# Performance work log

Measured on AMD Instinct MI355X. Metric: run time of the kernel, lower is better.

## Reference

```python
import jax, jax.numpy as jnp
import numpy as np

B, C, E, L = 128, 128, 10, 16  # atoms, channels, elements, num_ell (lmax=3)
K3_0, K2_0, K1_0 = 23, 4, 1    # num_params per correlation order, 0e output
K3_1, K2_1, K1_1 = 33, 6, 1    # num_params per correlation order, 1o output (num_equiv=3)


def setup_inputs() -> dict:
    key = jax.random.key(0)
    ks = jax.random.split(key, 16)
    inp = {
        'x': jax.random.normal(ks[0], (B, C, L), jnp.float32),
        'y': jax.random.uniform(ks[1], (B, E), jnp.float32),
        # generalized CG (U) buffers -- random dense stand-ins with faithful shapes
        'U1_0e': jax.random.normal(ks[2], (L, K1_0), jnp.float32),
        'U2_0e': jax.random.normal(ks[3], (L, L, K2_0), jnp.float32),
        'U3_0e': jax.random.normal(ks[4], (L, L, L, K3_0), jnp.float32),
        'U1_1o': jax.random.normal(ks[5], (3, L, K1_1), jnp.float32),
        'U2_1o': jax.random.normal(ks[6], (3, L, L, K2_1), jnp.float32),
        'U3_1o': jax.random.normal(ks[7], (3, L, L, L, K3_1), jnp.float32),
        # per-element weights, init randn/num_params as in torch
        'w1_0e': jax.random.normal(ks[8], (E, K1_0, C), jnp.float32) / K1_0,
        'w2_0e': jax.random.normal(ks[9], (E, K2_0, C), jnp.float32) / K2_0,
        'w3_0e': jax.random.normal(ks[10], (E, K3_0, C), jnp.float32) / K3_0,
        'w1_1o': jax.random.normal(ks[11], (E, K1_1, C), jnp.float32) / K1_1,
        'w2_1o': jax.random.normal(ks[12], (E, K2_1, C), jnp.float32) / K2_1,
        'w3_1o': jax.random.normal(ks[13], (E, K3_1, C), jnp.float32) / K3_1,
    }
    return inp


def _contract_0e(x, y, U1, U2, U3, w1, w2, w3):
    # main: 'wxik,ekc,bci,be->bcwx' (explicit path to control peak memory)
    wy3 = jnp.einsum('ekc,be->bkc', w3, y)              # [B,K3,C]
    t = jnp.einsum('wxik,bkc->bcwxi', U3, wy3)          # [B,C,L,L,L]
    out = jnp.einsum('bcwxi,bci->bcwx', t, x)           # [B,C,L,L]
    # order 2: weighting 'wxk,ekc,be->bcwx', features 'bcwi,bci->bcw'
    c2 = jnp.einsum('wxk,ekc,be->bcwx', U2, w2, y)
    out = jnp.einsum('bcwi,bci->bcw', c2 + out, x)
    # order 1: weighting 'wk,ekc,be->bcw', features 'bci,bci->bc'
    c1 = jnp.einsum('wk,ekc,be->bcw', U1, w1, y)
    out = jnp.einsum('bci,bci->bc', c1 + out, x)
    return out  # [B, C]


def _contract_1o(x, y, U1, U2, U3, w1, w2, w3):
    # main: 'wxvik,ekc,bci,be->bcwxv'  (w = equivariance dim of size 3)
    wy3 = jnp.einsum('ekc,be->bkc', w3, y)              # [B,K3,C]
    t = jnp.einsum('wxvik,bkc->bcwxvi', U3, wy3)        # [B,C,3,L,L,L]
    out = jnp.einsum('bcwxvi,bci->bcwxv', t, x)         # [B,C,3,L,L]
    # order 2: 'wxvk,ekc,be->bcwxv' ; features 'bcwxi,bci->bcwx'
    c2 = jnp.einsum('wxvk,ekc,be->bcwxv', U2, w2, y)
    out = jnp.einsum('bcwxi,bci->bcwx', c2 + out, x)
    # order 1: 'wxk,ekc,be->bcwx' ; features 'bcwi,bci->bcw'
    c1 = jnp.einsum('wxk,ekc,be->bcwx', U1, w1, y)
    out = jnp.einsum('bcwi,bci->bcw', c1 + out, x)
    return out.reshape(out.shape[0], -1)  # [B, 3*C]


def reference(x, y, U1_0e, U2_0e, U3_0e, U1_1o, U2_1o, U3_1o,
              w1_0e, w2_0e, w3_0e, w1_1o, w2_1o, w3_1o):
    out0 = _contract_0e(x, y, U1_0e, U2_0e, U3_0e, w1_0e, w2_0e, w3_0e)
    out1 = _contract_1o(x, y, U1_1o, U2_1o, U3_1o, w1_1o, w2_1o, w3_1o)
    return jnp.concatenate([out0, out1], axis=-1)  # [B, C + 3*C]
```

## Files before the change

kernel.cpp:

```cpp
#include <hip/hip_runtime.h>


typedef float  f32x4  __attribute__((ext_vector_type(4)));
typedef short  short8 __attribute__((ext_vector_type(8)));

namespace {
constexpr int EE = 10;

struct Sh1 {
  unsigned short B1[64][552];
  float x[16][64];
  float z[40][64];
  float red[12][64];
};
struct Sh0 {
  unsigned short B0[64][392];
  float x[16][64];
  float z[28][64];
  float red[8][64];
};
union ShU { Sh1 o1; Sh0 o0; };
}

__device__ __forceinline__ unsigned cvtpk(float lo, float hi) {
  unsigned r;
  asm("v_cvt_pk_bf16_f32 %0, %1, %2" : "=v"(r) : "v"(lo), "v"(hi));
  return r;
}

__device__ __forceinline__ short8 pack8(float f0, float f1, float f2, float f3,
                                        float f4, float f5, float f6, float f7) {
  union { short8 s; unsigned u[4]; } r;
  r.u[0] = cvtpk(f0, f1);
  r.u[1] = cvtpk(f2, f3);
  r.u[2] = cvtpk(f4, f5);
  r.u[3] = cvtpk(f6, f7);
  return r.s;
}

__global__ __launch_bounds__(768) void symcon_mfma(
    const float* __restrict__ x,
    const float* __restrict__ y,
    const float* __restrict__ U1_0e,
    const float* __restrict__ U2_0e,
    const float* __restrict__ U3_0e,
    const float* __restrict__ U1_1o,
    const float* __restrict__ U2_1o,
    const float* __restrict__ U3_1o,
    const float* __restrict__ w1_0e, const float* __restrict__ w2_0e,
    const float* __restrict__ w3_0e, const float* __restrict__ w1_1o,
    const float* __restrict__ w2_1o, const float* __restrict__ w3_1o,
    float* __restrict__ out)
{
  __shared__ ShU sh;

  const int tid   = threadIdx.x;
  const int blk   = blockIdx.x;
  const bool is1o = (blk < 256);
  const int pblk  = is1o ? blk : blk - 256;
  const int pair0 = pblk * 64;
  const int b     = pblk >> 1;
  const int lane  = tid & 63;
  const int wv    = tid >> 6;
  const int lrow  = lane & 15;
  const int lgr   = lane >> 4;

  if (is1o) {
    for (int t = tid; t < 16 * 64; t += 768) {
      const int i = t >> 6, n = t & 63;
      sh.o1.x[i][n] = x[(size_t)(pair0 + n) * 16 + i];
    }
    for (int t = tid; t < 40 * 64; t += 768) {
      const int n  = t & 63;
      const int zi = t >> 6;
      const int c  = ((pblk & 1) << 6) + n;
      const float* yb = y + b * EE;
      const float* wsrc; int stride;
      if      (zi < 33) { wsrc = w3_1o + zi * 128 + c;        stride = 33 * 128; }
      else if (zi < 39) { wsrc = w2_1o + (zi - 33) * 128 + c; stride =  6 * 128; }
      else              { wsrc = w1_1o + c;                   stride =      128; }
      float a = 0.f;
      #pragma unroll
      for (int e = 0; e < EE; ++e) a += wsrc[e * stride] * yb[e];
      sh.o1.z[zi][n] = a;
    }
    __syncthreads();

    #pragma unroll 1
    for (int idx = tid; idx < 272 * 64; idx += 768) {
      const int p = idx & 63, cp = idx >> 6;
      const int k0 = cp * 2;
      float v0, v1;
      if (k0 < 528) {
        const int i = k0 / 33, kk = k0 - i * 33;
        v0 = sh.o1.x[i][p] * sh.o1.z[kk][p];
        const int k1 = k0 + 1;
        const int i1 = k1 / 33, kk1 = k1 - i1 * 33;
        v1 = sh.o1.x[i1][p] * sh.o1.z[kk1][p];
      } else if (k0 < 534) {
        v0 = sh.o1.z[33 + (k0 - 528)][p];
        v1 = (k0 + 1 < 534) ? sh.o1.z[33 + (k0 - 527)][p] : 0.f;
      } else {
        v0 = 0.f; v1 = 0.f;
      }
      *(unsigned*)&sh.o1.B1[p][k0] = cvtpk(v0, v1);
    }
    __syncthreads();

    const int mbase = wv * 64;
    const float* __restrict__ U3r[4];
    #pragma unroll
    for (int mf = 0; mf < 4; ++mf)
      U3r[mf] = U3_1o + (size_t)(mbase + mf * 16 + lrow) * 528 + lgr * 8;

    f32x4 acc[4][4] = {};

    #pragma unroll 2
    for (int t = 0; t < 16; ++t) {
      short8 af[4];
      #pragma unroll
      for (int mf = 0; mf < 4; ++mf) {
        f32x4 a  = *(const f32x4*)(U3r[mf] + t * 32);
        f32x4 bq = *(const f32x4*)(U3r[mf] + t * 32 + 4);
        af[mf] = pack8(a[0], a[1], a[2], a[3], bq[0], bq[1], bq[2], bq[3]);
      }
      short8 bfr[4];
      #pragma unroll
      for (int nf = 0; nf < 4; ++nf)
        bfr[nf] = *(const short8*)&sh.o1.B1[nf * 16 + lrow][t * 32 + lgr * 8];
      #pragma unroll
      for (int mf = 0; mf < 4; ++mf)
        #pragma unroll
        for (int nf = 0; nf < 4; ++nf)
          acc[mf][nf] = __builtin_amdgcn_mfma_f32_16x16x32_bf16(af[mf], bfr[nf], acc[mf][nf], 0, 0, 0);
    }
    {
      short8 af[4];
      #pragma unroll
      for (int mf = 0; mf < 4; ++mf) {
        const int row = mbase + mf * 16 + lrow;
        if (lgr < 2) {
          const float* p = U3_1o + (size_t)row * 528 + 512 + lgr * 8;
          f32x4 a = *(const f32x4*)p; f32x4 bq = *(const f32x4*)(p + 4);
          af[mf] = pack8(a[0], a[1], a[2], a[3], bq[0], bq[1], bq[2], bq[3]);
        } else if (lgr == 2) {
          const float* p = U2_1o + row * 6;
          af[mf] = pack8(p[0], p[1], p[2], p[3], p[4], p[5], 0.f, 0.f);
        } else {
          af[mf] = short8{0, 0, 0, 0, 0, 0, 0, 0};
        }
      }
      short8 bfr[4];
      #pragma unroll
      for (int nf = 0; nf < 4; ++nf)
        bfr[nf] = *(const short8*)&sh.o1.B1[nf * 16 + lrow][512 + lgr * 8];
      #pragma unroll
      for (int mf = 0; mf < 4; ++mf)
        #pragma unroll
        for (int nf = 0; nf < 4; ++nf)
          acc[mf][nf] = __builtin_amdgcn_mfma_f32_16x16x32_bf16(af[mf], bfr[nf], acc[mf][nf], 0, 0, 0);
    }

    float s[4] = {0.f, 0.f, 0.f, 0.f};
    const int rg = lgr * 4;
    #pragma unroll
    for (int mf = 0; mf < 4; ++mf) {
      #pragma unroll
      for (int reg = 0; reg < 4; ++reg) {
        const int q  = (mbase + mf * 16 + rg + reg) & 255;
        const int qa = q >> 4, qb = q & 15;
        #pragma unroll
        for (int nf = 0; nf < 4; ++nf) {
          const int p = nf * 16 + lrow;
          s[nf] += acc[mf][nf][reg] * (sh.o1.x[qa][p] * sh.o1.x[qb][p]);
        }
      }
    }
    #pragma unroll
    for (int nf = 0; nf < 4; ++nf) {
      s[nf] += __shfl_xor(s[nf], 16);
      s[nf] += __shfl_xor(s[nf], 32);
    }
    if (lane < 16) {
      #pragma unroll
      for (int nf = 0; nf < 4; ++nf) sh.o1.red[wv][nf * 16 + lane] = s[nf];
    }
    __syncthreads();

    if (tid < 192) {
      const int slot = tid >> 6;
      const int n    = tid & 63;
      const int cc   = ((pblk & 1) << 6) + n;
      float v = sh.o1.red[4 * slot][n] + sh.o1.red[4 * slot + 1][n]
              + sh.o1.red[4 * slot + 2][n] + sh.o1.red[4 * slot + 3][n];
      float u1 = 0.f;
      #pragma unroll
      for (int xx = 0; xx < 16; ++xx) u1 += U1_1o[slot * 16 + xx] * sh.o1.x[xx][n];
      out[(size_t)b * 512 + 128 + cc * 3 + slot] = v + sh.o1.z[39][n] * u1;
    }
  } else {
    for (int t = tid; t < 16 * 64; t += 768) {
      const int i = t >> 6, n = t & 63;
      sh.o0.x[i][n] = x[(size_t)(pair0 + n) * 16 + i];
    }
    for (int t = tid; t < 28 * 64; t += 768) {
      const int n  = t & 63;
      const int zi = t >> 6;
      const int c  = ((pblk & 1) << 6) + n;
      const float* yb = y + b * EE;
      const float* wsrc; int stride;
      if      (zi < 23) { wsrc = w3_0e + zi * 128 + c;        stride = 23 * 128; }
      else if (zi < 27) { wsrc = w2_0e + (zi - 23) * 128 + c; stride =  4 * 128; }
      else              { wsrc = w1_0e + c;                   stride =      128; }
      float a = 0.f;
      #pragma unroll
      for (int e = 0; e < EE; ++e) a += wsrc[e * stride] * yb[e];
      sh.o0.z[zi][n] = a;
    }
    __syncthreads();

    #pragma unroll 1
    for (int idx = tid; idx < 192 * 64; idx += 768) {
      const int p = idx & 63, cp = idx >> 6;
      const int k0 = cp * 2;
      float v0, v1;
      if (k0 < 368) {
        const int i = k0 / 23, kk = k0 - i * 23;
        v0 = sh.o0.x[i][p] * sh.o0.z[kk][p];
        const int k1 = k0 + 1;
        const int i1 = k1 / 23, kk1 = k1 - i1 * 23;
        v1 = sh.o0.x[i1][p] * sh.o0.z[kk1][p];
      } else if (k0 < 372) {
        v0 = sh.o0.z[23 + (k0 - 368)][p];
        v1 = (k0 + 1 < 372) ? sh.o0.z[23 + (k0 - 367)][p] : 0.f;
      } else {
        v0 = 0.f; v1 = 0.f;
      }
      *(unsigned*)&sh.o0.B0[p][k0] = cvtpk(v0, v1);
    }
    __syncthreads();

    if (wv < 8) {
      const int mbase = wv * 32;
      const float* __restrict__ U3r[2];
      #pragma unroll
      for (int mf = 0; mf < 2; ++mf)
        U3r[mf] = U3_0e + (size_t)(mbase + mf * 16 + lrow) * 368 + lgr * 8;

      f32x4 acc[2][4] = {};

      #pragma unroll 2
      for (int t = 0; t < 11; ++t) {
        short8 af[2];
        #pragma unroll
        for (int mf = 0; mf < 2; ++mf) {
          f32x4 a  = *(const f32x4*)(U3r[mf] + t * 32);
          f32x4 bq = *(const f32x4*)(U3r[mf] + t * 32 + 4);
          af[mf] = pack8(a[0], a[1], a[2], a[3], bq[0], bq[1], bq[2], bq[3]);
        }
        short8 bfr[4];
        #pragma unroll
        for (int nf = 0; nf < 4; ++nf)
          bfr[nf] = *(const short8*)&sh.o0.B0[nf * 16 + lrow][t * 32 + lgr * 8];
        #pragma unroll
        for (int mf = 0; mf < 2; ++mf)
          #pragma unroll
          for (int nf = 0; nf < 4; ++nf)
            acc[mf][nf] = __builtin_amdgcn_mfma_f32_16x16x32_bf16(af[mf], bfr[nf], acc[mf][nf], 0, 0, 0);
      }
      {
        short8 af[2];
        #pragma unroll
        for (int mf = 0; mf < 2; ++mf) {
          const int row = mbase + mf * 16 + lrow;
          if (lgr < 2) {
            const float* p = U3_0e + (size_t)row * 368 + 352 + lgr * 8;
            f32x4 a = *(const f32x4*)p; f32x4 bq = *(const f32x4*)(p + 4);
            af[mf] = pack8(a[0], a[1], a[2], a[3], bq[0], bq[1], bq[2], bq[3]);
          } else if (lgr == 2) {
            const float* p = U2_0e + row * 4;
            af[mf] = pack8(p[0], p[1], p[2], p[3], 0.f, 0.f, 0.f, 0.f);
          } else {
            af[mf] = short8{0, 0, 0, 0, 0, 0, 0, 0};
          }
        }
        short8 bfr[4];
        #pragma unroll
        for (int nf = 0; nf < 4; ++nf)
          bfr[nf] = *(const short8*)&sh.o0.B0[nf * 16 + lrow][352 + lgr * 8];
        #pragma unroll
        for (int mf = 0; mf < 2; ++mf)
          #pragma unroll
          for (int nf = 0; nf < 4; ++nf)
            acc[mf][nf] = __builtin_amdgcn_mfma_f32_16x16x32_bf16(af[mf], bfr[nf], acc[mf][nf], 0, 0, 0);
      }

      float s[4] = {0.f, 0.f, 0.f, 0.f};
      const int rg = lgr * 4;
      #pragma unroll
      for (int mf = 0; mf < 2; ++mf) {
        #pragma unroll
        for (int reg = 0; reg < 4; ++reg) {
          const int q  = mbase + mf * 16 + rg + reg;
          const int qa = q >> 4, qb = q & 15;
          #pragma unroll
          for (int nf = 0; nf < 4; ++nf) {
            const int p = nf * 16 + lrow;
            s[nf] += acc[mf][nf][reg] * (sh.o0.x[qa][p] * sh.o0.x[qb][p]);
          }
        }
      }
      #pragma unroll
      for (int nf = 0; nf < 4; ++nf) {
        s[nf] += __shfl_xor(s[nf], 16);
        s[nf] += __shfl_xor(s[nf], 32);
      }
      if (lane < 16) {
        #pragma unroll
        for (int nf = 0; nf < 4; ++nf) sh.o0.red[wv][nf * 16 + lane] = s[nf];
      }
    }
    __syncthreads();

    if (tid < 64) {
      const int n  = tid;
      const int cc = ((pblk & 1) << 6) + n;
      float v = 0.f;
      #pragma unroll
      for (int k = 0; k < 8; ++k) v += sh.o0.red[k][n];
      float u1 = 0.f;
      #pragma unroll
      for (int xx = 0; xx < 16; ++xx) u1 += U1_0e[xx] * sh.o0.x[xx][n];
      out[(size_t)b * 512 + cc] = v + sh.o0.z[27][n] * u1;
    }
  }
}

extern "C" void kernel_launch(void* const* d_in, const int* in_sizes, int n_in,
                              void* d_out, int out_size, void* d_ws, size_t ws_size,
                              hipStream_t stream) {
  const float* x     = (const float*)d_in[0];
  const float* y     = (const float*)d_in[1];
  const float* U1_0e = (const float*)d_in[2];
  const float* U2_0e = (const float*)d_in[3];
  const float* U3_0e = (const float*)d_in[4];
  const float* U1_1o = (const float*)d_in[5];
  const float* U2_1o = (const float*)d_in[6];
  const float* U3_1o = (const float*)d_in[7];
  const float* w1_0e = (const float*)d_in[8];
  const float* w2_0e = (const float*)d_in[9];
  const float* w3_0e = (const float*)d_in[10];
  const float* w1_1o = (const float*)d_in[11];
  const float* w2_1o = (const float*)d_in[12];
  const float* w3_1o = (const float*)d_in[13];
  (void)in_sizes; (void)n_in; (void)out_size; (void)d_ws; (void)ws_size;

  hipLaunchKernelGGL(symcon_mfma, dim3(512), dim3(768), 0, stream,
                     x, y, U1_0e, U2_0e, U3_0e, U1_1o, U2_1o, U3_1o,
                     w1_0e, w2_0e, w3_0e, w1_1o, w2_1o, w3_1o,
                     (float*)d_out);
}
```

Before: 56.37 us.

## Split K-dimension staging into two LDS halves and interleave 1o/0e blocks

The bf16 B operand tile in shared memory is built and consumed in two K-halves instead of all at once, cutting the LDS footprint roughly in half so more workgroups can be resident per CU. Each half is built, synchronized, run through MFMA, then overwritten by the next half, which adds extra barriers. Block assignment is also changed so even blocks do the 1o work and odd blocks do the 0e work, interleaving heavy and light blocks across the grid.

Result: slower. 77.15 us (+36.9%).

```diff
diff --git a/kernel.cpp b/kernel.cpp
--- a/kernel.cpp
+++ b/kernel.cpp
@@ -7,19 +7,19 @@
 namespace {
 constexpr int EE = 10;
 
-struct Sh1 {
-  unsigned short B1[64][552];
+struct __attribute__((aligned(16))) Sh1 {
+  unsigned short B1[64][288];
   float x[16][64];
   float z[40][64];
   float red[12][64];
 };
-struct Sh0 {
-  unsigned short B0[64][392];
+struct __attribute__((aligned(16))) Sh0 {
+  unsigned short B0[64][192];
   float x[16][64];
   float z[28][64];
   float red[8][64];
 };
-union ShU { Sh1 o1; Sh0 o0; };
+union __attribute__((aligned(16))) ShU { Sh1 o1; Sh0 o0; };
 }
 
 __device__ __forceinline__ unsigned cvtpk(float lo, float hi) {
@@ -56,8 +56,8 @@
 
   const int tid   = threadIdx.x;
   const int blk   = blockIdx.x;
-  const bool is1o = (blk < 256);
-  const int pblk  = is1o ? blk : blk - 256;
+  const bool is1o = ((blk & 1) == 0);
+  const int pblk  = blk >> 1;
   const int pair0 = pblk * 64;
   const int b     = pblk >> 1;
   const int lane  = tid & 63;
@@ -87,22 +87,13 @@
     __syncthreads();
 
     #pragma unroll 1
-    for (int idx = tid; idx < 272 * 64; idx += 768) {
+    for (int idx = tid; idx < 144 * 64; idx += 768) {
       const int p = idx & 63, cp = idx >> 6;
       const int k0 = cp * 2;
-      float v0, v1;
-      if (k0 < 528) {
-        const int i = k0 / 33, kk = k0 - i * 33;
-        v0 = sh.o1.x[i][p] * sh.o1.z[kk][p];
-        const int k1 = k0 + 1;
-        const int i1 = k1 / 33, kk1 = k1 - i1 * 33;
-        v1 = sh.o1.x[i1][p] * sh.o1.z[kk1][p];
-      } else if (k0 < 534) {
-        v0 = sh.o1.z[33 + (k0 - 528)][p];
-        v1 = (k0 + 1 < 534) ? sh.o1.z[33 + (k0 - 527)][p] : 0.f;
-      } else {
-        v0 = 0.f; v1 = 0.f;
-      }
+      const int i0 = k0 / 33,       kk0 = k0 - i0 * 33;
+      const int i1 = (k0 + 1) / 33, kk1 = (k0 + 1) - i1 * 33;
+      const float v0 = sh.o1.x[i0][p] * sh.o1.z[kk0][p];
+      const float v1 = sh.o1.x[i1][p] * sh.o1.z[kk1][p];
       *(unsigned*)&sh.o1.B1[p][k0] = cvtpk(v0, v1);
     }
     __syncthreads();
@@ -116,12 +107,53 @@
     f32x4 acc[4][4] = {};
 
     #pragma unroll 2
-    for (int t = 0; t < 16; ++t) {
+    for (int t = 0; t < 9; ++t) {
       short8 af[4];
       #pragma unroll
       for (int mf = 0; mf < 4; ++mf) {
         f32x4 a  = *(const f32x4*)(U3r[mf] + t * 32);
         f32x4 bq = *(const f32x4*)(U3r[mf] + t * 32 + 4);
+        af[mf] = pack8(a[0], a[1], a[2], a[3], bq[0], bq[1], bq[2], bq[3]);
+      }
+      short8 bfr[4];
+      #pragma unroll
+      for (int nf = 0; nf < 4; ++nf)
+        bfr[nf] = *(const short8*)&sh.o1.B1[nf * 16 + lrow][t * 32 + lgr * 8];
+      #pragma unroll
+      for (int mf = 0; mf < 4; ++mf)
+        #pragma unroll
+        for (int nf = 0; nf < 4; ++nf)
+          acc[mf][nf] = __builtin_amdgcn_mfma_f32_16x16x32_bf16(af[mf], bfr[nf], acc[mf][nf], 0, 0, 0);
+    }
+    __syncthreads();
+
+    #pragma unroll 1
+    for (int idx = tid; idx < 128 * 64; idx += 768) {
+      const int p = idx & 63, cp = idx >> 6;
+      const int k0 = 288 + cp * 2;
+      float v0, v1;
+      if (k0 < 528) {
+        const int i0 = k0 / 33,       kk0 = k0 - i0 * 33;
+        const int i1 = (k0 + 1) / 33, kk1 = (k0 + 1) - i1 * 33;
+        v0 = sh.o1.x[i0][p] * sh.o1.z[kk0][p];
+        v1 = sh.o1.x[i1][p] * sh.o1.z[kk1][p];
+      } else if (k0 < 534) {
+        v0 = sh.o1.z[33 + (k0 - 528)][p];
+        v1 = sh.o1.z[33 + (k0 - 527)][p];
+      } else {
+        v0 = 0.f; v1 = 0.f;
+      }
+      *(unsigned*)&sh.o1.B1[p][k0 - 288] = cvtpk(v0, v1);
+    }
+    __syncthreads();
+
+    #pragma unroll 2
+    for (int t = 0; t < 7; ++t) {
+      short8 af[4];
+      #pragma unroll
+      for (int mf = 0; mf < 4; ++mf) {
+        f32x4 a  = *(const f32x4*)(U3r[mf] + 288 + t * 32);
+        f32x4 bq = *(const f32x4*)(U3r[mf] + 288 + t * 32 + 4);
         af[mf] = pack8(a[0], a[1], a[2], a[3], bq[0], bq[1], bq[2], bq[3]);
       }
       short8 bfr[4];
@@ -153,7 +185,7 @@
       short8 bfr[4];
       #pragma unroll
       for (int nf = 0; nf < 4; ++nf)
-        bfr[nf] = *(const short8*)&sh.o1.B1[nf * 16 + lrow][512 + lgr * 8];
+        bfr[nf] = *(const short8*)&sh.o1.B1[nf * 16 + lrow][224 + lgr * 8];
       #pragma unroll
       for (int mf = 0; mf < 4; ++mf)
         #pragma unroll
@@ -220,42 +252,76 @@
     __syncthreads();
 
     #pragma unroll 1
-    for (int idx = tid; idx < 192 * 64; idx += 768) {
+    for (int idx = tid; idx < 96 * 64; idx += 768) {
       const int p = idx & 63, cp = idx >> 6;
       const int k0 = cp * 2;
+      const int i0 = k0 / 23,       kk0 = k0 - i0 * 23;
+      const int i1 = (k0 + 1) / 23, kk1 = (k0 + 1) - i1 * 23;
+      const float v0 = sh.o0.x[i0][p] * sh.o0.z[kk0][p];
+      const float v1 = sh.o0.x[i1][p] * sh.o0.z[kk1][p];
+      *(unsigned*)&sh.o0.B0[p][k0] = cvtpk(v0, v1);
+    }
+    __syncthreads();
+
+    const int mbase = wv * 32;
+    const float* __restrict__ U3r[2];
+    #pragma unroll
+    for (int mf = 0; mf < 2; ++mf)
+      U3r[mf] = U3_0e + (size_t)(mbase + mf * 16 + lrow) * 368 + lgr * 8;
+
+    f32x4 acc[2][4] = {};
+
+    if (wv < 8) {
+      #pragma unroll 2
+      for (int t = 0; t < 6; ++t) {
+        short8 af[2];
+        #pragma unroll
+        for (int mf = 0; mf < 2; ++mf) {
+          f32x4 a  = *(const f32x4*)(U3r[mf] + t * 32);
+          f32x4 bq = *(const f32x4*)(U3r[mf] + t * 32 + 4);
+          af[mf] = pack8(a[0], a[1], a[2], a[3], bq[0], bq[1], bq[2], bq[3]);
+        }
+        short8 bfr[4];
+        #pragma unroll
+        for (int nf = 0; nf < 4; ++nf)
+          bfr[nf] = *(const short8*)&sh.o0.B0[nf * 16 + lrow][t * 32 + lgr * 8];
+        #pragma unroll
+        for (int mf = 0; mf < 2; ++mf)
+          #pragma unroll
+          for (int nf = 0; nf < 4; ++nf)
+            acc[mf][nf] = __builtin_amdgcn_mfma_f32_16x16x32_bf16(af[mf], bfr[nf], acc[mf][nf], 0, 0, 0);
+      }
+    }
+    __syncthreads();
+
+    #pragma unroll 1
+    for (int idx = tid; idx < 96 * 64; idx += 768) {
+      const int p = idx & 63, cp = idx >> 6;
+      const int k0 = 192 + cp * 2;
       float v0, v1;
       if (k0 < 368) {
-        const int i = k0 / 23, kk = k0 - i * 23;
-        v0 = sh.o0.x[i][p] * sh.o0.z[kk][p];
-        const int k1 = k0 + 1;
-        const int i1 = k1 / 23, kk1 = k1 - i1 * 23;
+        const int i0 = k0 / 23,       kk0 = k0 - i0 * 23;
+        const int i1 = (k0 + 1) / 23, kk1 = (k0 + 1) - i1 * 23;
+        v0 = sh.o0.x[i0][p] * sh.o0.z[kk0][p];
         v1 = sh.o0.x[i1][p] * sh.o0.z[kk1][p];
       } else if (k0 < 372) {
         v0 = sh.o0.z[23 + (k0 - 368)][p];
-        v1 = (k0 + 1 < 372) ? sh.o0.z[23 + (k0 - 367)][p] : 0.f;
+        v1 = sh.o0.z[23 + (k0 - 367)][p];
       } else {
         v0 = 0.f; v1 = 0.f;
       }
-      *(unsigned*)&sh.o0.B0[p][k0] = cvtpk(v0, v1);
+      *(unsigned*)&sh.o0.B0[p][k0 - 192] = cvtpk(v0, v1);
     }
     __syncthreads();
 
     if (wv < 8) {
-      const int mbase = wv * 32;
-      const float* __restrict__ U3r[2];
-      #pragma unroll
-      for (int mf = 0; mf < 2; ++mf)
-        U3r[mf] = U3_0e + (size_t)(mbase + mf * 16 + lrow) * 368 + lgr * 8;
-
-      f32x4 acc[2][4] = {};
-
       #pragma unroll 2
-      for (int t = 0; t < 11; ++t) {
+      for (int t = 0; t < 5; ++t) {
         short8 af[2];
         #pragma unroll
         for (int mf = 0; mf < 2; ++mf) {
-          f32x4 a  = *(const f32x4*)(U3r[mf] + t * 32);
-          f32x4 bq = *(const f32x4*)(U3r[mf] + t * 32 + 4);
+          f32x4 a  = *(const f32x4*)(U3r[mf] + 192 + t * 32);
+          f32x4 bq = *(const f32x4*)(U3r[mf] + 192 + t * 32 + 4);
           af[mf] = pack8(a[0], a[1], a[2], a[3], bq[0], bq[1], bq[2], bq[3]);
         }
         short8 bfr[4];
@@ -287,7 +353,7 @@
         short8 bfr[4];
         #pragma unroll
         for (int nf = 0; nf < 4; ++nf)
-          bfr[nf] = *(const short8*)&sh.o0.B0[nf * 16 + lrow][352 + lgr * 8];
+          bfr[nf] = *(const short8*)&sh.o0.B0[nf * 16 + lrow][160 + lgr * 8];
         #pragma unroll
         for (int mf = 0; mf < 2; ++mf)
           #pragma unroll
```
